# Performance work log

Measured on AMD Instinct MI355X. Metric: run time of the kernel, lower is better.

Reference implementation:

```python
import jax, jax.numpy as jnp
import numpy as np

B, S, E, H, V, C = 512, 64, 512, 1024, 1024, 1000
PAD = 0

def setup_inputs() -> dict:
    key = jax.random.key(0)
    ks = jax.random.split(key, 10)
    x_in = jax.random.randint(ks[0], (B, S), 0, V)
    x_lengths = jax.random.randint(ks[1], (B,), 1, S + 1)
    emb_w = jax.random.normal(ks[2], (V, E), jnp.float32) * 0.02
    emb_w = emb_w.at[PAD].set(0.0)  # padding_idx row is zero
    s_h = 1.0 / np.sqrt(H)
    w_ih = jax.random.uniform(ks[3], (H, E), jnp.float32, -s_h, s_h)
    b_ih = jax.random.uniform(ks[4], (H,), jnp.float32, -s_h, s_h)
    w_hh = jax.random.uniform(ks[5], (H, H), jnp.float32, -s_h, s_h)
    b_hh = jax.random.uniform(ks[6], (H,), jnp.float32, -s_h, s_h)
    fc1_w = jax.random.uniform(ks[7], (H, H), jnp.float32, -s_h, s_h)
    fc1_b = jnp.zeros((H,), jnp.float32)
    fc2_w = jax.random.uniform(ks[8], (C, H), jnp.float32, -s_h, s_h)
    fc2_b = jnp.zeros((C,), jnp.float32)
    return dict(x_in=x_in, x_lengths=x_lengths, emb_w=emb_w, w_ih=w_ih, b_ih=b_ih,
                w_hh=w_hh, b_hh=b_hh, fc1_w=fc1_w, fc1_b=fc1_b, fc2_w=fc2_w, fc2_b=fc2_b)

def reference(x_in, x_lengths, emb_w, w_ih, b_ih, w_hh, b_hh, fc1_w, fc1_b, fc2_w, fc2_b):
    # Embedding lookup: [B,S,E]
    x_emb = emb_w[x_in]
    # Precompute input projections for all steps: [S,B,H]
    x_proj = jnp.einsum('bse,he->sbh', x_emb, w_ih) + b_ih
    def step(h, xp):
        h_new = jnp.tanh(xp + h @ w_hh.T + b_hh)
        return h_new, h_new
    h0 = jnp.zeros((x_in.shape[0], w_hh.shape[0]), x_proj.dtype)
    _, hs = jax.lax.scan(step, h0, x_proj)          # [S,B,H]
    y_out = jnp.transpose(hs, (1, 0, 2))            # [B,S,H]
    # column_gather: final valid hidden per sequence
    idx = (x_lengths - 1).astype(jnp.int32)
    y_last = jnp.take_along_axis(y_out, idx[:, None, None], axis=1)[:, 0, :]  # [B,H]
    # dropout in eval mode = identity
    y = jax.nn.relu(y_last @ fc1_w.T + fc1_b)
    y = y @ fc2_w.T + fc2_b
    return y
```

## Files before the change

### kernel.cpp

```cpp
#include <hip/hip_runtime.h>
#include <hip/hip_bf16.h>
#include <stdint.h>
#include <stddef.h>

#define B_SZ 512
#define S_SZ 64
#define E_SZ 512
#define H_SZ 1024
#define V_SZ 1024
#define C_SZ 1000

typedef __hip_bfloat16 bf16;
typedef __attribute__((ext_vector_type(8))) __bf16 bf16x8;
typedef __attribute__((ext_vector_type(4))) float f32x4;

#define EMB_OFF   (0ull)
#define WIH_OFF   (1ull << 20)
#define WHH_OFF   (2ull << 20)
#define FC1_OFF   (4ull << 20)
#define FC2_OFF   (6ull << 20)
#define HB_OFF    (8ull << 20)
#define XP_OFF    (12ull << 20)
#define BAR_OFF   (FC2_OFF + 2048000ull)

__device__ __forceinline__ void gl_lds16(const void* g, void* l) {
  __builtin_amdgcn_global_load_lds(
      (const __attribute__((address_space(1))) unsigned int*)g,
      (__attribute__((address_space(3))) unsigned int*)l, 16, 0, 0);
}

__global__ __launch_bounds__(256) void prep_kernel(
    const float* __restrict__ emb_w, const float* __restrict__ w_ih,
    const float* __restrict__ w_hh, const float* __restrict__ fc1_w,
    const float* __restrict__ fc2_w, char* __restrict__ ws) {
  bf16* emb = (bf16*)(ws + EMB_OFF);
  bf16* wih = (bf16*)(ws + WIH_OFF);
  bf16* whh = (bf16*)(ws + WHH_OFF);
  bf16* fc1 = (bf16*)(ws + FC1_OFF);
  bf16* fc2 = (bf16*)(ws + FC2_OFF);
  bf16* h0  = (bf16*)(ws + HB_OFF);

  const long N_EMB = 524288, N_WIH = 524288, N_WHH = 1048576;
  const long N_FC1 = 1048576, N_FC2 = 1048576, N_H0 = 524288;
  const long TOTAL = N_EMB + N_WIH + N_WHH + N_FC1 + N_FC2 + N_H0;

  long stride = (long)gridDim.x * blockDim.x;
  for (long i = (long)blockIdx.x * blockDim.x + threadIdx.x; i < TOTAL; i += stride) {
    long j = i;
    if (j < N_EMB) {
      emb[j] = (j < E_SZ) ? __float2bfloat16(0.f) : __float2bfloat16(emb_w[j]);
      continue;
    }
    j -= N_EMB;
    if (j < N_WIH) { wih[j] = __float2bfloat16(w_ih[j]); continue; }
    j -= N_WIH;
    if (j < N_WHH) { whh[j] = __float2bfloat16(w_hh[j]); continue; }
    j -= N_WHH;
    if (j < N_FC1) { fc1[j] = __float2bfloat16(fc1_w[j]); continue; }
    j -= N_FC1;
    if (j < N_FC2) {
      fc2[j] = (j < (long)C_SZ * H_SZ) ? __float2bfloat16(fc2_w[j]) : __float2bfloat16(0.f);
      continue;
    }
    j -= N_FC2;
    h0[j] = __float2bfloat16(0.f);
  }
}

__global__ __launch_bounds__(256) void xproj_kernel(
    const int* __restrict__ x_in, const float* __restrict__ b_ih,
    char* __restrict__ ws) {
  const bf16* emb = (const bf16*)(ws + EMB_OFF);
  const bf16* wih = (const bf16*)(ws + WIH_OFF);
  bf16* xp = (bf16*)(ws + XP_OFF);

  __shared__ bf16 Asm[2][128][64];
  __shared__ bf16 Bsm[2][128][64];

  const int tid = threadIdx.x;
  const int lane = tid & 63;
  const int wid = tid >> 6;
  const int mb = blockIdx.x >> 3;
  const int nb = blockIdx.x & 7;
  const int rowBase = mb * 128;
  const int colBase = nb * 128;
  const int s = rowBase >> 9;

  const int lrow = lane >> 3;
  const int lchk = lane & 7;

  int tok[4];
#pragma unroll
  for (int i = 0; i < 4; ++i) {
    int rt = wid * 32 + i * 8 + lrow;
    int b = (rowBase + rt) & 511;
    tok[i] = x_in[b * S_SZ + s];
  }

  const int wr = wid >> 1, wc = wid & 1;
  f32x4 acc[4][4];
#pragma unroll
  for (int i = 0; i < 4; ++i)
#pragma unroll
    for (int j = 0; j < 4; ++j) acc[i][j] = (f32x4){0.f, 0.f, 0.f, 0.f};

  auto stage = [&](int buf, int k0) {
#pragma unroll
    for (int i = 0; i < 4; ++i) {
      int rt = wid * 32 + i * 8;
      int sc = (lchk ^ ((rt + lrow) & 7)) * 8;
      gl_lds16(emb + (size_t)tok[i] * E_SZ + k0 + sc, &Asm[buf][rt][0]);
    }
#pragma unroll
    for (int i = 0; i < 4; ++i) {
      int rt = wid * 32 + i * 8;
      int sc = (lchk ^ ((rt + lrow) & 7)) * 8;
      gl_lds16(wih + (size_t)(colBase + rt + lrow) * E_SZ + k0 + sc, &Bsm[buf][rt][0]);
    }
  };

  stage(0, 0);
  __syncthreads();
  int cur = 0;
  for (int t8 = 0; t8 < 8; ++t8) {
    if (t8 < 7) stage(cur ^ 1, (t8 + 1) * 64);
#pragma unroll
    for (int kk = 0; kk < 2; ++kk) {
      const int kfc = kk * 4 + (lane >> 4);
      bf16x8 a[4], b[4];
#pragma unroll
      for (int i = 0; i < 4; ++i) {
        int r = wr * 64 + i * 16 + (lane & 15);
        a[i] = *(const bf16x8*)&Asm[cur][r][(kfc ^ (r & 7)) * 8];
      }
#pragma unroll
      for (int j = 0; j < 4; ++j) {
        int r = wc * 64 + j * 16 + (lane & 15);
        b[j] = *(const bf16x8*)&Bsm[cur][r][(kfc ^ (r & 7)) * 8];
      }
#pragma unroll
      for (int i = 0; i < 4; ++i)
#pragma unroll
        for (int j = 0; j < 4; ++j)
          acc[i][j] = __builtin_amdgcn_mfma_f32_16x16x32_bf16(a[i], b[j], acc[i][j], 0, 0, 0);
    }
    __syncthreads();
    cur ^= 1;
  }

  const int crow = (lane >> 4) * 4;
  const int ccol = lane & 15;
#pragma unroll
  for (int j = 0; j < 4; ++j) {
    const int col = colBase + wc * 64 + j * 16 + ccol;
    const float bias = b_ih[col];
#pragma unroll
    for (int i = 0; i < 4; ++i) {
      const int r0 = rowBase + wr * 64 + i * 16 + crow;
#pragma unroll
      for (int reg = 0; reg < 4; ++reg) {
        float v = acc[i][j][reg] + bias;
        xp[(size_t)(r0 + reg) * H_SZ + col] = __float2bfloat16(v);
      }
    }
  }
}

__device__ __forceinline__ void clusterbar(unsigned* bar, unsigned target, bool acq) {
  __syncthreads();
  if (threadIdx.x == 0) {
    __hip_atomic_fetch_add(bar, 1u, __ATOMIC_RELEASE, __HIP_MEMORY_SCOPE_AGENT);
    while (__hip_atomic_load(bar, __ATOMIC_RELAXED, __HIP_MEMORY_SCOPE_AGENT) < target)
      __builtin_amdgcn_s_sleep(1);
    if (acq)
      (void)__hip_atomic_load(bar, __ATOMIC_ACQUIRE, __HIP_MEMORY_SCOPE_AGENT);
  }
  asm volatile("" ::: "memory");
  __syncthreads();
}

__device__ __forceinline__ void load_breg(bf16x8 (&breg)[16][2],
                                          const bf16* w, int c0, int lane) {
  const bf16* wrow = w + (size_t)c0 * H_SZ + ((lane >> 4) << 3);
#pragma unroll
  for (int i = 0; i < 16; ++i)
#pragma unroll
    for (int kk = 0; kk < 2; ++kk)
      breg[i][kk] = *(const bf16x8*)(wrow + i * 64 + kk * 32);
}

template <int MODE>
__device__ __forceinline__ void phase(
    const bf16* __restrict__ Asrc, const bf16x8 (&breg)[16][2], bf16* Ap,
    int lane, int wid, int rowBase, float bias_v,
    const bf16 (&xv)[4], const int (&lenv)[4], int t, int r0, int c0,
    bf16* __restrict__ dst, bf16* __restrict__ yl, float* __restrict__ outf) {
  const int wr = wid & 1;
  f32x4 acc = (f32x4){0.f, 0.f, 0.f, 0.f};

  const bf16* sbase = Asrc +
      (size_t)(rowBase + (wid & 1) * 16 + (lane & 15)) * H_SZ +
      (wid >> 1) * 32 + ((lane >> 4) << 3);
  bf16* sdst0 = Ap + ((wid & 1) * 2 + (wid >> 1)) * 512;

  if (wid < 4) {
    gl_lds16(sbase, sdst0);
    asm volatile("" ::: "memory");
    gl_lds16(sbase + 64, sdst0 + 2048);
    asm volatile("" ::: "memory");
    gl_lds16(sbase + 128, sdst0 + 2 * 2048);
  }

#pragma unroll
  for (int i = 0; i < 16; ++i) {
    if (wid < 4) {
      if (i < 14)       asm volatile("s_waitcnt vmcnt(2)" ::: "memory");
      else if (i == 14) asm volatile("s_waitcnt vmcnt(1)" ::: "memory");
      else              asm volatile("s_waitcnt vmcnt(0)" ::: "memory");
    }
    __builtin_amdgcn_s_barrier();
    asm volatile("" ::: "memory");
    if (wid < 4 && i < 13)
      gl_lds16(sbase + (i + 3) * 64, sdst0 + ((i + 3) & 3) * 2048);
    const bf16* Ab = Ap + (i & 3) * 2048 + wr * 1024 + lane * 8;
    bf16x8 a0 = *(const bf16x8*)(Ab);
    bf16x8 a1 = *(const bf16x8*)(Ab + 512);
    acc = __builtin_amdgcn_mfma_f32_16x16x32_bf16(a0, breg[i][0], acc, 0, 0, 0);
    acc = __builtin_amdgcn_mfma_f32_16x16x32_bf16(a1, breg[i][1], acc, 0, 0, 0);
  }

#pragma unroll
  for (int reg = 0; reg < 4; ++reg) {
    const int row = r0 + reg;
    float v = acc[reg];
    if constexpr (MODE == 0) {
      v += bias_v + __bfloat162float(xv[reg]);
      v = fminf(fmaxf(v, -15.f), 15.f);
      float e = __expf(2.f * v);
      float h = (e - 1.f) / (e + 1.f);
      bf16 hb = __float2bfloat16(h);
      dst[(size_t)row * H_SZ + c0] = hb;
      if (t == lenv[reg] - 1) yl[(size_t)row * H_SZ + c0] = hb;
    } else if constexpr (MODE == 1) {
      dst[(size_t)row * H_SZ + c0] = __float2bfloat16(fmaxf(v + bias_v, 0.f));
    } else {
      if (c0 < C_SZ) outf[(size_t)row * C_SZ + c0] = v + bias_v;
    }
  }
}

__global__ __launch_bounds__(512, 2) void rnn_fused_kernel(
    const float* __restrict__ b_hh, const float* __restrict__ fc1_b,
    const float* __restrict__ fc2_b, const int* __restrict__ lens,
    char* __restrict__ ws, float* __restrict__ out) {
  __shared__ bf16 Ap[8192];

  const int tid = threadIdx.x;
  const int lane = tid & 63, wid = tid >> 6;
  const int bid = blockIdx.x;
  const int mb = ((bid & 7) << 1) | ((bid >> 3) & 1);
  const int nb = bid >> 4;
  const int rowBase = mb * 32;
  const int colBase = nb * 64;
  const int wr = wid & 1, wc = wid >> 1;
  const int r0 = rowBase + wr * 16 + ((lane >> 4) << 2);
  const int c0 = colBase + wc * 16 + (lane & 15);

  const bf16* whh  = (const bf16*)(ws + WHH_OFF);
  const bf16* fc1w = (const bf16*)(ws + FC1_OFF);
  const bf16* fc2w = (const bf16*)(ws + FC2_OFF);
  const bf16* xp   = (const bf16*)(ws + XP_OFF);
  bf16* hb = (bf16*)(ws + HB_OFF);
  bf16* yl = (bf16*)(ws + EMB_OFF);
  bf16* y1 = (bf16*)(ws + WIH_OFF);
  unsigned* bar = (unsigned*)(ws + BAR_OFF + (size_t)mb * 128);

  const float bhv = b_hh[c0];
  int lenv[4];
#pragma unroll
  for (int reg = 0; reg < 4; ++reg) lenv[reg] = lens[r0 + reg];

  bf16x8 breg[16][2];
  load_breg(breg, whh, c0, lane);

  bf16 xv[4];
#pragma unroll
  for (int reg = 0; reg < 4; ++reg) xv[reg] = xp[(size_t)(r0 + reg) * H_SZ + c0];

#pragma unroll 1
  for (int t = 0; t < S_SZ; ++t) {
    const bf16* hsrc = hb + ((size_t)(t & 3) << 19);
    bf16* hdst = hb + ((size_t)((t + 1) & 3) << 19);
    phase<0>(hsrc, breg, Ap, lane, wid, rowBase, bhv, xv, lenv, t, r0, c0,
             hdst, yl, nullptr);
    if (t < S_SZ - 1) {
      const bf16* xpn = xp + (size_t)(t + 1) * (B_SZ * H_SZ);
#pragma unroll
      for (int reg = 0; reg < 4; ++reg)
        xv[reg] = xpn[(size_t)(r0 + reg) * H_SZ + c0];
    }
    clusterbar(bar, (unsigned)(t + 1) * 16u, (t & 3) == 3);
  }

  load_breg(breg, fc1w, c0, lane);
  const float b1v = fc1_b[c0];
  phase<1>(yl, breg, Ap, lane, wid, rowBase, b1v, xv, lenv, 0, r0, c0,
           y1, nullptr, nullptr);
  clusterbar(bar, 65u * 16u, true);

  load_breg(breg, fc2w, c0, lane);
  const float b2v = (c0 < C_SZ) ? fc2_b[c0] : 0.f;
  phase<2>(y1, breg, Ap, lane, wid, rowBase, b2v, xv, lenv, 0, r0, c0,
           nullptr, nullptr, out);
}

extern "C" void kernel_launch(void* const* d_in, const int* in_sizes, int n_in,
                              void* d_out, int out_size, void* d_ws, size_t ws_size,
                              hipStream_t stream) {
  (void)in_sizes; (void)n_in; (void)out_size; (void)ws_size;
  const int* x_in = (const int*)d_in[0];
  const int* x_len = (const int*)d_in[1];
  const float* emb_w = (const float*)d_in[2];
  const float* w_ih = (const float*)d_in[3];
  const float* b_ih = (const float*)d_in[4];
  const float* w_hh = (const float*)d_in[5];
  const float* b_hh = (const float*)d_in[6];
  const float* fc1_w = (const float*)d_in[7];
  const float* fc1_b = (const float*)d_in[8];
  const float* fc2_w = (const float*)d_in[9];
  const float* fc2_b = (const float*)d_in[10];
  char* ws = (char*)d_ws;
  float* out = (float*)d_out;

  prep_kernel<<<2048, 256, 0, stream>>>(emb_w, w_ih, w_hh, fc1_w, fc2_w, ws);

  xproj_kernel<<<2048, 256, 0, stream>>>(x_in, b_ih, ws);

  rnn_fused_kernel<<<256, 512, 0, stream>>>(b_hh, fc1_b, fc2_b, x_len, ws, out);
}
```

Measured before the change: 629.7 us.

## Load full A tile into LDS at once instead of 4-stage ring pipeline

Each recurrent phase now has all 8 waves issue global-to-LDS loads for the whole 32x1024 bf16 A tile up front, then wait once and barrier once before running all MFMAs out of LDS. This replaces the 4-slot ring buffer, in which only 4 waves loaded and a barrier ran on every k-iteration. An empty asm keeps the preloaded weight registers alive so the compiler cannot rematerialize them. The cost is 64KB of LDS per block instead of 16KB, which may affect occupancy under the 2-blocks-per-CU launch bound, and load latency is no longer overlapped with compute.

```diff
diff --git a/kernel.cpp b/kernel.cpp
--- a/kernel.cpp
+++ b/kernel.cpp
@@ -27,6 +27,11 @@
   __builtin_amdgcn_global_load_lds(
       (const __attribute__((address_space(1))) unsigned int*)g,
       (__attribute__((address_space(3))) unsigned int*)l, 16, 0, 0);
+}
+
+__device__ __forceinline__ void keep(bf16x8& v) {
+  f32x4& f = reinterpret_cast<f32x4&>(v);
+  asm volatile("" : "+v"(f));
 }
 
 __global__ __launch_bounds__(256) void prep_kernel(
@@ -185,8 +190,10 @@
 #pragma unroll
   for (int i = 0; i < 16; ++i)
 #pragma unroll
-    for (int kk = 0; kk < 2; ++kk)
+    for (int kk = 0; kk < 2; ++kk) {
       breg[i][kk] = *(const bf16x8*)(wrow + i * 64 + kk * 32);
+      keep(breg[i][kk]);
+    }
 }
 
 template <int MODE>
@@ -195,36 +202,30 @@
     int lane, int wid, int rowBase, float bias_v,
     const bf16 (&xv)[4], const int (&lenv)[4], int t, int r0, int c0,
     bf16* __restrict__ dst, bf16* __restrict__ yl, float* __restrict__ outf) {
+  const int lr = lane & 15;
+  const int lk = (lane >> 4) << 3;
+  const int fbase = wid * 8;
+
+#pragma unroll
+  for (int o = 0; o < 8; ++o) {
+    const int f = fbase + o;
+    const int rowhalf = f >> 5;
+    const int kchunk = f & 31;
+    const bf16* g = Asrc + (size_t)(rowBase + rowhalf * 16 + lr) * H_SZ +
+                    kchunk * 32 + lk;
+    gl_lds16(g, Ap + f * 512);
+  }
+  asm volatile("s_waitcnt vmcnt(0)" ::: "memory");
+  __builtin_amdgcn_s_barrier();
+  __builtin_amdgcn_sched_barrier(0);
+
   const int wr = wid & 1;
   f32x4 acc = (f32x4){0.f, 0.f, 0.f, 0.f};
-
-  const bf16* sbase = Asrc +
-      (size_t)(rowBase + (wid & 1) * 16 + (lane & 15)) * H_SZ +
-      (wid >> 1) * 32 + ((lane >> 4) << 3);
-  bf16* sdst0 = Ap + ((wid & 1) * 2 + (wid >> 1)) * 512;
-
-  if (wid < 4) {
-    gl_lds16(sbase, sdst0);
-    asm volatile("" ::: "memory");
-    gl_lds16(sbase + 64, sdst0 + 2048);
-    asm volatile("" ::: "memory");
-    gl_lds16(sbase + 128, sdst0 + 2 * 2048);
-  }
-
+  const bf16* Abase = Ap + (wr * 32) * 512 + lane * 8;
 #pragma unroll
   for (int i = 0; i < 16; ++i) {
-    if (wid < 4) {
-      if (i < 14)       asm volatile("s_waitcnt vmcnt(2)" ::: "memory");
-      else if (i == 14) asm volatile("s_waitcnt vmcnt(1)" ::: "memory");
-      else              asm volatile("s_waitcnt vmcnt(0)" ::: "memory");
-    }
-    __builtin_amdgcn_s_barrier();
-    asm volatile("" ::: "memory");
-    if (wid < 4 && i < 13)
-      gl_lds16(sbase + (i + 3) * 64, sdst0 + ((i + 3) & 3) * 2048);
-    const bf16* Ab = Ap + (i & 3) * 2048 + wr * 1024 + lane * 8;
-    bf16x8 a0 = *(const bf16x8*)(Ab);
-    bf16x8 a1 = *(const bf16x8*)(Ab + 512);
+    bf16x8 a0 = *(const bf16x8*)(Abase + (2 * i) * 512);
+    bf16x8 a1 = *(const bf16x8*)(Abase + (2 * i + 1) * 512);
     acc = __builtin_amdgcn_mfma_f32_16x16x32_bf16(a0, breg[i][0], acc, 0, 0, 0);
     acc = __builtin_amdgcn_mfma_f32_16x16x32_bf16(a1, breg[i][1], acc, 0, 0, 0);
   }
@@ -253,7 +254,7 @@
     const float* __restrict__ b_hh, const float* __restrict__ fc1_b,
     const float* __restrict__ fc2_b, const int* __restrict__ lens,
     char* __restrict__ ws, float* __restrict__ out) {
-  __shared__ bf16 Ap[8192];
+  __shared__ bf16 Ap[32768];
 
   const int tid = threadIdx.x;
   const int lane = tid & 63, wid = tid >> 6;
```

Result: slower. 761.2 us (+20.9%).
